# Kernel optimization log

Hardware: AMD Instinct MI355X
Metric: run time of the kernel (lower is better)

The kernel has to match this reference:

```python
import jax, jax.numpy as jnp
import numpy as np

RATE = 2          # attention_rate from __init__
SOFTMAX_SCALE = 10.0  # standard contextual-attention temperature
EPS = 1e-8


def setup_inputs() -> dict:
    key = jax.random.key(0)
    k1, k2 = jax.random.split(key)
    x = jax.random.normal(k1, (1, 128, 192, 192), dtype=jnp.float32)
    # binary hole mask: 1 = hole (to be filled), 0 = valid background
    mask = (jax.random.uniform(k2, (1, 1, 192, 192)) < 0.25).astype(jnp.float32)
    return {"x": x, "mask": mask}


def reference(x, mask):
    b, c, h, w = x.shape
    r = RATE
    hs, ws = h // r, w // r
    n = hs * ws

    # F.interpolate(..., mode='nearest') downsample == strided slice when divisible
    xs = x[:, :, ::r, ::r]            # [b, c, hs, ws]
    ms = mask[:, :, ::r, ::r]         # [b, 1, hs, ws]

    feat = xs.reshape(b, c, n)        # queries (raw) and keys (normalized)
    keys = feat / (jnp.sqrt(jnp.sum(feat * feat, axis=1, keepdims=True)) + EPS)

    # conv-based correlation == all-pairs inner product with normalized bg patches
    scores = jnp.einsum('bcn,bcm->bnm', feat, keys) * SOFTMAX_SCALE  # [b, n, n]

    valid = (ms.reshape(b, 1, n) == 0.0)  # background key locations
    scores = jnp.where(valid, scores, -1e4)
    attn = jax.nn.softmax(scores, axis=-1)
    attn = attn * valid                   # zero out hole keys exactly

    # extract non-overlapping r x r patches from full-res x: [b, n, c*r*r]
    patches = (x.reshape(b, c, hs, r, ws, r)
                 .transpose(0, 2, 4, 1, 3, 5)
                 .reshape(b, n, c * r * r))

    # transposed-conv reconstruction == weighted sum of patches, folded back
    recon = jnp.einsum('bnm,bmd->bnd', attn, patches)   # [b, n, c*r*r]
    recon_img = (recon.reshape(b, hs, ws, c, r, r)
                      .transpose(0, 3, 1, 4, 2, 5)
                      .reshape(b, c, h, w))

    # composite: keep known pixels, fill holes with attended reconstruction
    return x * (1.0 - mask) + recon_img * mask
```

## Files before the change

kernel.cpp:

```cpp
#include <hip/hip_runtime.h>
#include <hip/hip_bf16.h>

typedef _Float16 f16x8 __attribute__((ext_vector_type(8)));
typedef _Float16 f16x4 __attribute__((ext_vector_type(4)));
typedef float    f32x4 __attribute__((ext_vector_type(4)));

#define HW   36864
#define W_   192
#define NS   9216
#define CCH  128
#define DV   512
#define ROWS 64
#define KV   64
#define NT   144
#define SPL  4
#define KT   (NT / SPL)

__global__ __launch_bounds__(256) void prep_vt_kernel(const float* __restrict__ x,
        _Float16* __restrict__ Vt, _Float16* __restrict__ F16)
{
    int m = blockIdx.x * 256 + threadIdx.x;
    int d = blockIdx.y;
    int c = d >> 2, di = (d >> 1) & 1, dj = d & 1;
    int i = m / 96, j = m - i * 96;
    float v = x[c * HW + (2 * i + di) * W_ + (2 * j + dj)];
    _Float16 h = (_Float16)v;
    Vt[(size_t)d * NS + m] = h;
    if ((d & 3) == 0) F16[m * CCH + c] = h;
}

__global__ __launch_bounds__(64) void prep_csv_kernel(const _Float16* __restrict__ F16,
        const float* __restrict__ mask, float* __restrict__ csv)
{
    int m = blockIdx.x;
    int t = threadIdx.x;
    float a = (float)F16[m * CCH + 2 * t];
    float b = (float)F16[m * CCH + 2 * t + 1];
    float ss = a * a + b * b;
    #pragma unroll
    for (int off = 1; off <= 32; off <<= 1)
        ss += __shfl_xor(ss, off);
    if (t == 0) {
        int i = m / 96, j = m - i * 96;
        float ms = mask[(2 * i) * W_ + 2 * j];
        csv[m] = (ms == 0.0f) ? 10.0f / (sqrtf(ss) + 1e-8f) : 0.0f;
    }
}

__global__ __launch_bounds__(256, 2) void flash_kernel(const _Float16* __restrict__ F16,
        const _Float16* __restrict__ Vt, const float* __restrict__ csv,
        _Float16* __restrict__ po, float* __restrict__ av)
{
    __shared__ _Float16 Kbuf[2][KV * CCH];
    __shared__ _Float16 Pbuf[2][ROWS * KV];
    __shared__ float    abuf[2][ROWS];
    __shared__ float    lbuf[ROWS];
    __shared__ int      flagbuf[KT];

    const int tid  = threadIdx.x;
    const int wv   = tid >> 6;
    const int lane = tid & 63;
    const int g    = lane >> 4, c16 = lane & 15;
    const int n0   = (blockIdx.x >> 1) * ROWS;
    const int d0   = (blockIdx.x & 1) * 256;
    const int sp   = blockIdx.y;
    const int t0   = sp * KT;

    if (tid < KT) flagbuf[tid] = 0;

    f16x8 q[4];
    #pragma unroll
    for (int kk = 0; kk < 4; ++kk)
        q[kk] = *(const f16x8*)(F16 + (n0 + wv * 16 + c16) * CCH + kk * 32 + g * 8);

    f32x4 o[4][4];
    #pragma unroll
    for (int rf = 0; rf < 4; ++rf)
        #pragma unroll
        for (int df = 0; df < 4; ++df) o[rf][df] = 0.0f;
    float m_run[4], l_run[4];
    #pragma unroll
    for (int r = 0; r < 4; ++r) { m_run[r] = -1e30f; l_run[r] = 0.0f; }

    const int kkey = tid >> 2;
    const int kch0 = (tid & 3) * 4;

    {
        const _Float16* ks = F16 + (size_t)(t0 * KV + kkey) * CCH + kch0 * 8;
        #pragma unroll
        for (int j = 0; j < 4; ++j)
            *(f16x8*)(&Kbuf[0][kkey * CCH + (((kch0 + j) ^ (kkey & 7)) * 8)])
                = *(const f16x8*)(ks + j * 8);
    }
    asm volatile("s_waitcnt lgkmcnt(0)" ::: "memory");
    __builtin_amdgcn_s_barrier();

    for (int tl = 0; tl < KT; ++tl) {
        const int buf = tl & 1;
        const int m0  = (t0 + tl) * KV;

        f16x8 kpre[4];
        const bool havek = (tl + 1 < KT);
        if (havek) {
            const _Float16* ks = F16 + (size_t)((t0 + tl + 1) * KV + kkey) * CCH + kch0 * 8;
            #pragma unroll
            for (int j = 0; j < 4; ++j) kpre[j] = *(const f16x8*)(ks + j * 8);
        }
        f16x8 vreg[8];
        #pragma unroll
        for (int kf = 0; kf < 2; ++kf)
            #pragma unroll
            for (int df = 0; df < 4; ++df)
                vreg[kf * 4 + df] = *(const f16x8*)(Vt
                    + (size_t)(d0 + wv * 64 + df * 16 + c16) * NS + m0 + kf * 32 + g * 8);

        f32x4 s[4];
        #pragma unroll
        for (int cf = 0; cf < 4; ++cf) s[cf] = 0.0f;
        #pragma unroll
        for (int cf = 0; cf < 4; ++cf) {
            const int key = cf * 16 + c16;
            const _Float16* kr = &Kbuf[buf][key * CCH];
            const int sw = key & 7;
            #pragma unroll
            for (int kk = 0; kk < 4; ++kk)
                s[cf] = __builtin_amdgcn_mfma_f32_16x16x32_f16(
                            q[kk], *(const f16x8*)(kr + (((kk * 4 + g) ^ sw) * 8)), s[cf], 0, 0, 0);
        }

        float cs[4];
        #pragma unroll
        for (int cf = 0; cf < 4; ++cf) cs[cf] = csv[m0 + cf * 16 + c16];

        float sv[4][4], tm[4];
        #pragma unroll
        for (int r = 0; r < 4; ++r) tm[r] = -1e30f;
        #pragma unroll
        for (int cf = 0; cf < 4; ++cf)
            #pragma unroll
            for (int r = 0; r < 4; ++r) {
                float val = (cs[cf] > 0.0f) ? s[cf][r] * cs[cf] : -1e30f;
                sv[cf][r] = val;
                tm[r] = fmaxf(tm[r], val);
            }
        #pragma unroll
        for (int r = 0; r < 4; ++r)
            #pragma unroll
            for (int off = 1; off <= 8; off <<= 1)
                tm[r] = fmaxf(tm[r], __shfl_xor(tm[r], off));

        float al[4] = {1.0f, 1.0f, 1.0f, 1.0f};
        bool need = false;
        #pragma unroll
        for (int r = 0; r < 4; ++r) need = need || (tm[r] > m_run[r] + 8.0f);
        if (__any(need)) {
            #pragma unroll
            for (int r = 0; r < 4; ++r) {
                float nm = fmaxf(m_run[r], tm[r]);
                al[r] = __expf(m_run[r] - nm);
                l_run[r] *= al[r]; m_run[r] = nm;
            }
            if (lane == 0) flagbuf[tl] = 1;
        }
        if (c16 == 0) {
            #pragma unroll
            for (int r = 0; r < 4; ++r) abuf[buf][wv * 16 + g * 4 + r] = al[r];
        }

        float ps[4] = {0.0f, 0.0f, 0.0f, 0.0f};
        #pragma unroll
        for (int cf = 0; cf < 4; ++cf)
            #pragma unroll
            for (int r = 0; r < 4; ++r) {
                float e = (cs[cf] > 0.0f) ? __expf(sv[cf][r] - m_run[r]) : 0.0f;
                ps[r] += e;
                const int row = wv * 16 + g * 4 + r, key = cf * 16 + c16;
                Pbuf[buf][row * KV + (((key >> 3) ^ (row & 7)) * 8) + (key & 7)]
                    = (_Float16)e;
            }
        #pragma unroll
        for (int r = 0; r < 4; ++r) {
            #pragma unroll
            for (int off = 1; off <= 8; off <<= 1)
                ps[r] += __shfl_xor(ps[r], off);
            l_run[r] += ps[r];
        }

        if (havek) {
            #pragma unroll
            for (int j = 0; j < 4; ++j)
                *(f16x8*)(&Kbuf[buf ^ 1][kkey * CCH + (((kch0 + j) ^ (kkey & 7)) * 8)])
                    = kpre[j];
        }

        asm volatile("s_waitcnt lgkmcnt(0)" ::: "memory");
        __builtin_amdgcn_s_barrier();

        if (flagbuf[tl]) {
            #pragma unroll
            for (int rf = 0; rf < 4; ++rf) {
                f32x4 a4 = *(const f32x4*)(&abuf[buf][rf * 16 + g * 4]);
                #pragma unroll
                for (int df = 0; df < 4; ++df)
                    #pragma unroll
                    for (int r = 0; r < 4; ++r) o[rf][df][r] *= a4[r];
            }
        }
        #pragma unroll
        for (int kf = 0; kf < 2; ++kf) {
            f16x8 pa[4];
            #pragma unroll
            for (int rf = 0; rf < 4; ++rf) {
                const int row = rf * 16 + c16;
                pa[rf] = *(const f16x8*)(&Pbuf[buf][row * KV + (((kf * 4 + g) ^ (row & 7)) * 8)]);
            }
            #pragma unroll
            for (int df = 0; df < 4; ++df)
                #pragma unroll
                for (int rf = 0; rf < 4; ++rf)
                    o[rf][df] = __builtin_amdgcn_mfma_f32_16x16x32_f16(
                                    pa[rf], vreg[kf * 4 + df], o[rf][df], 0, 0, 0);
        }
    }

    if (c16 == 0) {
        #pragma unroll
        for (int r = 0; r < 4; ++r) {
            lbuf[wv * 16 + g * 4 + r] = (l_run[r] > 0.0f) ? 1.0f / l_run[r] : 0.0f;
            if (d0 == 0)
                av[sp * NS + n0 + wv * 16 + g * 4 + r] =
                    (l_run[r] > 0.0f) ? m_run[r] + __logf(l_run[r]) : -1e30f;
        }
    }
    asm volatile("s_waitcnt lgkmcnt(0)" ::: "memory");
    __builtin_amdgcn_s_barrier();

    #pragma unroll
    for (int rf = 0; rf < 4; ++rf) {
        f32x4 li = *(const f32x4*)(&lbuf[rf * 16 + g * 4]);
        #pragma unroll
        for (int df = 0; df < 4; ++df) {
            f16x4 res;
            #pragma unroll
            for (int r = 0; r < 4; ++r) res[r] = (_Float16)(o[rf][df][r] * li[r]);
            *(f16x4*)(po + ((size_t)sp * DV + d0 + wv * 64 + df * 16 + c16) * NS
                          + n0 + rf * 16 + g * 4) = res;
        }
    }
}

template<int S>
__global__ __launch_bounds__(192) void combine_kernel(const float* __restrict__ x,
        const float* __restrict__ mask, const _Float16* __restrict__ po,
        const float* __restrict__ av, float* __restrict__ out)
{
    int i = blockIdx.x;
    int c = blockIdx.y;
    int w = threadIdx.x;
    int n = i * 96 + (w >> 1);

    float A = -1e30f;
    #pragma unroll
    for (int s = 0; s < S; ++s) A = fmaxf(A, av[s * NS + n]);
    float wt[S], wsum = 0.0f;
    #pragma unroll
    for (int s = 0; s < S; ++s) {
        float a = av[s * NS + n];
        float e = (a > -1e29f) ? __expf(a - A) : 0.0f;
        wt[s] = e; wsum += e;
    }
    float invw = (wsum > 0.0f) ? 1.0f / wsum : 0.0f;

    #pragma unroll
    for (int di = 0; di < 2; ++di) {
        int h = 2 * i + di;
        int d = c * 4 + di * 2 + (w & 1);
        float rv = 0.0f;
        #pragma unroll
        for (int s = 0; s < S; ++s)
            rv += wt[s] * (float)po[((size_t)s * DV + d) * NS + n];
        rv *= invw;
        float xv = x[c * HW + h * W_ + w];
        float mv = mask[h * W_ + w];
        out[c * HW + h * W_ + w] = xv * (1.0f - mv) + rv * mv;
    }
}

extern "C" void kernel_launch(void* const* d_in, const int* in_sizes, int n_in,
                              void* d_out, int out_size, void* d_ws, size_t ws_size,
                              hipStream_t stream) {
    const float* x    = (const float*)d_in[0];
    const float* mask = (const float*)d_in[1];
    float* out = (float*)d_out;

    char* ws = (char*)d_ws;
    _Float16* Vt  = (_Float16*)(ws);
    _Float16* F16 = (_Float16*)(ws + 9437184);
    float*    csv = (float*)   (ws + 11796480);
    float*    av  = (float*)   (ws + 11833344);
    _Float16* po  = (_Float16*)(ws + 12128256);

    prep_vt_kernel <<<dim3(36, 512), 256, 0, stream>>>(x, Vt, F16);
    prep_csv_kernel<<<NS, 64, 0, stream>>>(F16, mask, csv);
    flash_kernel   <<<dim3(288, SPL), 256, 0, stream>>>(F16, Vt, csv, po, av);
    combine_kernel<SPL><<<dim3(96, 128), 192, 0, stream>>>(x, mask, po, av, out);
}
```

Baseline: 317.7 us.

## Warp-specialize flash kernel into softmax producers and PV consumers with async K loads

Splits the flash attention block into 8 waves: four compute QK^T scores and softmax into LDS, while four others stage the next K tile with global_load_lds and run the P·V MMAs for the previous tile one step behind. S and P are computed transposed, so each lane owns one row and the row reductions shrink to two cross-lane shuffles. The split count goes from 4 to 8 when the workspace allows, which adds more partial outputs for the combine kernel. The aim is to overlap softmax with the PV matmul and raise parallelism, at the cost of extra partial-output traffic and a barrier per tile.

Result: slower. 611.9 us (+92.6%).

```diff
diff --git a/kernel.cpp b/kernel.cpp
--- a/kernel.cpp
+++ b/kernel.cpp
@@ -13,8 +13,13 @@
 #define ROWS 64
 #define KV   64
 #define NT   144
-#define SPL  4
-#define KT   (NT / SPL)
+#define PROW 72
+
+__device__ __forceinline__ void gload_lds16(const _Float16* src, _Float16* dst) {
+    __builtin_amdgcn_global_load_lds(
+        (const __attribute__((address_space(1))) void*)src,
+        (__attribute__((address_space(3))) void*)dst, 16, 0, 0);
+}
 
 __global__ __launch_bounds__(256) void prep_vt_kernel(const float* __restrict__ x,
         _Float16* __restrict__ Vt, _Float16* __restrict__ F16)
@@ -47,15 +52,15 @@
     }
 }
 
-__global__ __launch_bounds__(256, 2) void flash_kernel(const _Float16* __restrict__ F16,
+template<int KT>
+__global__ __launch_bounds__(512, 4) void flash_kernel(const _Float16* __restrict__ F16,
         const _Float16* __restrict__ Vt, const float* __restrict__ csv,
         _Float16* __restrict__ po, float* __restrict__ av)
 {
-    __shared__ _Float16 Kbuf[2][KV * CCH];
-    __shared__ _Float16 Pbuf[2][ROWS * KV];
-    __shared__ float    abuf[2][ROWS];
-    __shared__ float    lbuf[ROWS];
-    __shared__ int      flagbuf[KT];
+    __shared__ __align__(16) _Float16 Kb[2][KV * CCH];
+    __shared__ __align__(16) _Float16 Pb[2][ROWS * PROW];
+    __shared__ __align__(16) float    abuf[2][ROWS];
+    __shared__ __align__(16) float    lbuf[ROWS];
 
     const int tid  = threadIdx.x;
     const int wv   = tid >> 6;
@@ -65,186 +70,152 @@
     const int d0   = (blockIdx.x & 1) * 256;
     const int sp   = blockIdx.y;
     const int t0   = sp * KT;
-
-    if (tid < KT) flagbuf[tid] = 0;
+    const bool prod = (wv < 4);
+    const int cw   = wv & 3;
+
+    auto stageK = [&](int buf, int t) {
+        #pragma unroll
+        for (int j = 0; j < 4; ++j) {
+            const int keyb = cw * 16 + j * 4;
+            const int key  = keyb + g;
+            const int sc   = (c16 & 8) | ((c16 & 7) ^ (key & 7));
+            gload_lds16(F16 + (size_t)(t * KV + key) * CCH + sc * 8,
+                        &Kb[buf][keyb * CCH]);
+        }
+    };
 
     f16x8 q[4];
-    #pragma unroll
-    for (int kk = 0; kk < 4; ++kk)
-        q[kk] = *(const f16x8*)(F16 + (n0 + wv * 16 + c16) * CCH + kk * 32 + g * 8);
-
+    float m_run = -1e30f, l_run = 0.0f;
+    if (prod) {
+        #pragma unroll
+        for (int kk = 0; kk < 4; ++kk)
+            q[kk] = *(const f16x8*)(F16 + (n0 + cw * 16 + c16) * CCH + kk * 32 + g * 8);
+    }
     f32x4 o[4][4];
     #pragma unroll
     for (int rf = 0; rf < 4; ++rf)
         #pragma unroll
         for (int df = 0; df < 4; ++df) o[rf][df] = 0.0f;
-    float m_run[4], l_run[4];
-    #pragma unroll
-    for (int r = 0; r < 4; ++r) { m_run[r] = -1e30f; l_run[r] = 0.0f; }
-
-    const int kkey = tid >> 2;
-    const int kch0 = (tid & 3) * 4;
-
-    {
-        const _Float16* ks = F16 + (size_t)(t0 * KV + kkey) * CCH + kch0 * 8;
-        #pragma unroll
-        for (int j = 0; j < 4; ++j)
-            *(f16x8*)(&Kbuf[0][kkey * CCH + (((kch0 + j) ^ (kkey & 7)) * 8)])
-                = *(const f16x8*)(ks + j * 8);
-    }
-    asm volatile("s_waitcnt lgkmcnt(0)" ::: "memory");
-    __builtin_amdgcn_s_barrier();
+
+    auto consume = [&](int tp) {
+        const int pb = tp & 1;
+        const int m0 = (t0 + tp) * KV;
+        #pragma unroll
+        for (int rf = 0; rf < 4; ++rf) {
+            f32x4 a4 = *(const f32x4*)(&abuf[pb][rf * 16 + g * 4]);
+            #pragma unroll
+            for (int df = 0; df < 4; ++df)
+                #pragma unroll
+                for (int r = 0; r < 4; ++r) o[rf][df][r] *= a4[r];
+        }
+        #pragma unroll
+        for (int kf = 0; kf < 2; ++kf) {
+            f16x8 vr[4];
+            #pragma unroll
+            for (int df = 0; df < 4; ++df)
+                vr[df] = *(const f16x8*)(Vt + (size_t)(d0 + cw * 64 + df * 16 + c16) * NS
+                                         + m0 + kf * 32 + g * 8);
+            f16x8 pa[4];
+            #pragma unroll
+            for (int rf = 0; rf < 4; ++rf)
+                pa[rf] = *(const f16x8*)(&Pb[pb][(rf * 16 + c16) * PROW + kf * 32 + g * 8]);
+            #pragma unroll
+            for (int df = 0; df < 4; ++df)
+                #pragma unroll
+                for (int rf = 0; rf < 4; ++rf)
+                    o[rf][df] = __builtin_amdgcn_mfma_f32_16x16x32_f16(
+                                    pa[rf], vr[df], o[rf][df], 0, 0, 0);
+        }
+    };
+
+    if (!prod) stageK(0, t0);
+    __syncthreads();
 
     for (int tl = 0; tl < KT; ++tl) {
         const int buf = tl & 1;
-        const int m0  = (t0 + tl) * KV;
-
-        f16x8 kpre[4];
-        const bool havek = (tl + 1 < KT);
-        if (havek) {
-            const _Float16* ks = F16 + (size_t)((t0 + tl + 1) * KV + kkey) * CCH + kch0 * 8;
-            #pragma unroll
-            for (int j = 0; j < 4; ++j) kpre[j] = *(const f16x8*)(ks + j * 8);
-        }
-        f16x8 vreg[8];
-        #pragma unroll
-        for (int kf = 0; kf < 2; ++kf)
-            #pragma unroll
-            for (int df = 0; df < 4; ++df)
-                vreg[kf * 4 + df] = *(const f16x8*)(Vt
-                    + (size_t)(d0 + wv * 64 + df * 16 + c16) * NS + m0 + kf * 32 + g * 8);
-
-        f32x4 s[4];
-        #pragma unroll
-        for (int cf = 0; cf < 4; ++cf) s[cf] = 0.0f;
-        #pragma unroll
-        for (int cf = 0; cf < 4; ++cf) {
-            const int key = cf * 16 + c16;
-            const _Float16* kr = &Kbuf[buf][key * CCH];
-            const int sw = key & 7;
-            #pragma unroll
-            for (int kk = 0; kk < 4; ++kk)
-                s[cf] = __builtin_amdgcn_mfma_f32_16x16x32_f16(
-                            q[kk], *(const f16x8*)(kr + (((kk * 4 + g) ^ sw) * 8)), s[cf], 0, 0, 0);
-        }
-
-        float cs[4];
-        #pragma unroll
-        for (int cf = 0; cf < 4; ++cf) cs[cf] = csv[m0 + cf * 16 + c16];
-
-        float sv[4][4], tm[4];
-        #pragma unroll
-        for (int r = 0; r < 4; ++r) tm[r] = -1e30f;
-        #pragma unroll
-        for (int cf = 0; cf < 4; ++cf)
-            #pragma unroll
-            for (int r = 0; r < 4; ++r) {
-                float val = (cs[cf] > 0.0f) ? s[cf][r] * cs[cf] : -1e30f;
-                sv[cf][r] = val;
-                tm[r] = fmaxf(tm[r], val);
-            }
-        #pragma unroll
-        for (int r = 0; r < 4; ++r)
-            #pragma unroll
-            for (int off = 1; off <= 8; off <<= 1)
-                tm[r] = fmaxf(tm[r], __shfl_xor(tm[r], off));
-
-        float al[4] = {1.0f, 1.0f, 1.0f, 1.0f};
-        bool need = false;
-        #pragma unroll
-        for (int r = 0; r < 4; ++r) need = need || (tm[r] > m_run[r] + 8.0f);
-        if (__any(need)) {
-            #pragma unroll
-            for (int r = 0; r < 4; ++r) {
-                float nm = fmaxf(m_run[r], tm[r]);
-                al[r] = __expf(m_run[r] - nm);
-                l_run[r] *= al[r]; m_run[r] = nm;
-            }
-            if (lane == 0) flagbuf[tl] = 1;
-        }
-        if (c16 == 0) {
-            #pragma unroll
-            for (int r = 0; r < 4; ++r) abuf[buf][wv * 16 + g * 4 + r] = al[r];
-        }
-
-        float ps[4] = {0.0f, 0.0f, 0.0f, 0.0f};
-        #pragma unroll
-        for (int cf = 0; cf < 4; ++cf)
-            #pragma unroll
-            for (int r = 0; r < 4; ++r) {
-                float e = (cs[cf] > 0.0f) ? __expf(sv[cf][r] - m_run[r]) : 0.0f;
-                ps[r] += e;
-                const int row = wv * 16 + g * 4 + r, key = cf * 16 + c16;
-                Pbuf[buf][row * KV + (((key >> 3) ^ (row & 7)) * 8) + (key & 7)]
-                    = (_Float16)e;
-            }
-        #pragma unroll
-        for (int r = 0; r < 4; ++r) {
-            #pragma unroll
-            for (int off = 1; off <= 8; off <<= 1)
-                ps[r] += __shfl_xor(ps[r], off);
-            l_run[r] += ps[r];
-        }
-
-        if (havek) {
-            #pragma unroll
-            for (int j = 0; j < 4; ++j)
-                *(f16x8*)(&Kbuf[buf ^ 1][kkey * CCH + (((kch0 + j) ^ (kkey & 7)) * 8)])
-                    = kpre[j];
-        }
-
-        asm volatile("s_waitcnt lgkmcnt(0)" ::: "memory");
-        __builtin_amdgcn_s_barrier();
-
-        if (flagbuf[tl]) {
-            #pragma unroll
-            for (int rf = 0; rf < 4; ++rf) {
-                f32x4 a4 = *(const f32x4*)(&abuf[buf][rf * 16 + g * 4]);
-                #pragma unroll
-                for (int df = 0; df < 4; ++df)
-                    #pragma unroll
-                    for (int r = 0; r < 4; ++r) o[rf][df][r] *= a4[r];
-            }
-        }
-        #pragma unroll
-        for (int kf = 0; kf < 2; ++kf) {
-            f16x8 pa[4];
-            #pragma unroll
-            for (int rf = 0; rf < 4; ++rf) {
-                const int row = rf * 16 + c16;
-                pa[rf] = *(const f16x8*)(&Pbuf[buf][row * KV + (((kf * 4 + g) ^ (row & 7)) * 8)]);
-            }
-            #pragma unroll
-            for (int df = 0; df < 4; ++df)
-                #pragma unroll
-                for (int rf = 0; rf < 4; ++rf)
-                    o[rf][df] = __builtin_amdgcn_mfma_f32_16x16x32_f16(
-                                    pa[rf], vreg[kf * 4 + df], o[rf][df], 0, 0, 0);
-        }
-    }
-
-    if (c16 == 0) {
-        #pragma unroll
-        for (int r = 0; r < 4; ++r) {
-            lbuf[wv * 16 + g * 4 + r] = (l_run[r] > 0.0f) ? 1.0f / l_run[r] : 0.0f;
-            if (d0 == 0)
-                av[sp * NS + n0 + wv * 16 + g * 4 + r] =
-                    (l_run[r] > 0.0f) ? m_run[r] + __logf(l_run[r]) : -1e30f;
-        }
-    }
-    asm volatile("s_waitcnt lgkmcnt(0)" ::: "memory");
-    __builtin_amdgcn_s_barrier();
-
-    #pragma unroll
-    for (int rf = 0; rf < 4; ++rf) {
-        f32x4 li = *(const f32x4*)(&lbuf[rf * 16 + g * 4]);
-        #pragma unroll
-        for (int df = 0; df < 4; ++df) {
-            f16x4 res;
-            #pragma unroll
-            for (int r = 0; r < 4; ++r) res[r] = (_Float16)(o[rf][df][r] * li[r]);
-            *(f16x4*)(po + ((size_t)sp * DV + d0 + wv * 64 + df * 16 + c16) * NS
-                          + n0 + rf * 16 + g * 4) = res;
+        if (prod) {
+            const int m0 = (t0 + tl) * KV;
+            f32x4 s[4];
+            #pragma unroll
+            for (int cf = 0; cf < 4; ++cf) s[cf] = 0.0f;
+            const int sw = c16 & 7;
+            #pragma unroll
+            for (int cf = 0; cf < 4; ++cf) {
+                const _Float16* kr = &Kb[buf][(cf * 16 + c16) * CCH];
+                #pragma unroll
+                for (int kk = 0; kk < 4; ++kk) {
+                    const int ch  = kk * 4 + g;
+                    const int sch = (ch & 8) | ((ch & 7) ^ sw);
+                    s[cf] = __builtin_amdgcn_mfma_f32_16x16x32_f16(
+                                *(const f16x8*)(kr + sch * 8), q[kk], s[cf], 0, 0, 0);
+                }
+            }
+            f32x4 cs4[4];
+            #pragma unroll
+            for (int cf = 0; cf < 4; ++cf)
+                cs4[cf] = *(const f32x4*)(csv + m0 + cf * 16 + g * 4);
+            float sv[4][4], tm = -1e30f;
+            #pragma unroll
+            for (int cf = 0; cf < 4; ++cf)
+                #pragma unroll
+                for (int r = 0; r < 4; ++r) {
+                    float c = cs4[cf][r];
+                    float v = (c > 0.0f) ? s[cf][r] * c : -1e30f;
+                    sv[cf][r] = v;
+                    tm = fmaxf(tm, v);
+                }
+            tm = fmaxf(tm, __shfl_xor(tm, 16));
+            tm = fmaxf(tm, __shfl_xor(tm, 32));
+            float al = 1.0f;
+            if (__any(tm > m_run + 8.0f)) {
+                float nm = fmaxf(m_run, tm);
+                al = __expf(m_run - nm);
+                l_run *= al; m_run = nm;
+            }
+            if (g == 0) abuf[buf][cw * 16 + c16] = al;
+            float ps = 0.0f;
+            #pragma unroll
+            for (int cf = 0; cf < 4; ++cf) {
+                f16x4 ph;
+                #pragma unroll
+                for (int r = 0; r < 4; ++r) {
+                    float c = cs4[cf][r];
+                    float e = (c > 0.0f) ? __expf(sv[cf][r] - m_run) : 0.0f;
+                    ps += e;
+                    ph[r] = (_Float16)e;
+                }
+                *(f16x4*)(&Pb[buf][(cw * 16 + c16) * PROW + cf * 16 + g * 4]) = ph;
+            }
+            ps += __shfl_xor(ps, 16);
+            ps += __shfl_xor(ps, 32);
+            l_run += ps;
+        } else {
+            if (tl + 1 < KT) stageK((tl + 1) & 1, t0 + tl + 1);
+            if (tl > 0) consume(tl - 1);
+        }
+        __syncthreads();
+    }
+
+    if (prod && g == 0) {
+        lbuf[cw * 16 + c16] = (l_run > 0.0f) ? 1.0f / l_run : 0.0f;
+        if (d0 == 0)
+            av[sp * NS + n0 + cw * 16 + c16] =
+                (l_run > 0.0f) ? m_run + __logf(l_run) : -1e30f;
+    }
+    __syncthreads();
+    if (!prod) {
+        consume(KT - 1);
+        #pragma unroll
+        for (int rf = 0; rf < 4; ++rf) {
+            f32x4 li = *(const f32x4*)(&lbuf[rf * 16 + g * 4]);
+            #pragma unroll
+            for (int df = 0; df < 4; ++df) {
+                f16x4 res;
+                #pragma unroll
+                for (int r = 0; r < 4; ++r) res[r] = (_Float16)(o[rf][df][r] * li[r]);
+                *(f16x4*)(po + ((size_t)sp * DV + d0 + cw * 64 + df * 16 + c16) * NS
+                              + n0 + rf * 16 + g * 4) = res;
+            }
         }
     }
 }
@@ -302,6 +273,13 @@
 
     prep_vt_kernel <<<dim3(36, 512), 256, 0, stream>>>(x, Vt, F16);
     prep_csv_kernel<<<NS, 64, 0, stream>>>(F16, mask, csv);
-    flash_kernel   <<<dim3(288, SPL), 256, 0, stream>>>(F16, Vt, csv, po, av);
-    combine_kernel<SPL><<<dim3(96, 128), 192, 0, stream>>>(x, mask, po, av, out);
-}
+
+    const size_t base = 12128256ull;
+    if (ws_size >= base + 8ull * 9437184ull) {
+        flash_kernel<18><<<dim3(288, 8), 512, 0, stream>>>(F16, Vt, csv, po, av);
+        combine_kernel<8><<<dim3(96, 128), 192, 0, stream>>>(x, mask, po, av, out);
+    } else {
+        flash_kernel<36><<<dim3(288, 4), 512, 0, stream>>>(F16, Vt, csv, po, av);
+        combine_kernel<4><<<dim3(96, 128), 192, 0, stream>>>(x, mask, po, av, out);
+    }
+}
```
